# Kernel tuning notes

Measured on AMD Instinct MI355X. Metric: run time of the kernel, lower is better.

The kernel has to match this reference:

```python
import jax, jax.numpy as jnp
from jax import lax
import numpy as np

B, DIM, L_IN = 8, 512, 4096
SCALE = 2
KSIZE = 17
DN = ('NCH', 'OIH', 'NCH')  # conv1d dimension numbers


def _aa_kernel(kernel_size: int, scale: int) -> np.ndarray:
    # replicates scipy.signal.kaiser_atten / kaiser_beta / windows.kaiser
    atten = 2.285 * (kernel_size - 1) * np.pi * (1.0 / scale) + 7.95
    if atten > 50:
        beta = 0.1102 * (atten - 8.7)
    elif atten > 21:
        beta = 0.5842 * (atten - 21) ** 0.4 + 0.07886 * (atten - 21)
    else:
        beta = 0.0
    win = np.kaiser(kernel_size, beta)
    xk = np.arange(kernel_size) - kernel_size // 2
    k = np.sinc(xk / scale) * win  # normalized sinc, same as torch.sinc
    return (k / k.sum()).astype(np.float32)


def setup_inputs() -> dict:
    key = jax.random.key(0)
    k1, k2, k3, k4, k5 = jax.random.split(key, 5)
    kconv = 2 * SCALE - 1
    return {
        'x': jax.random.normal(k1, (B, DIM, L_IN), dtype=jnp.float32),
        'conv_w': jax.random.normal(k2, (DIM, DIM, kconv), dtype=jnp.float32) * (1.0 / np.sqrt(DIM * kconv)),
        'conv_b': jax.random.normal(k3, (DIM,), dtype=jnp.float32) * 0.01,
        'aa_kernel': jnp.asarray(_aa_kernel(KSIZE, SCALE)),
        'proj_w': jax.random.normal(k4, (DIM, DIM), dtype=jnp.float32) * (1.0 / np.sqrt(DIM)),
        'proj_b': jax.random.normal(k5, (DIM,), dtype=jnp.float32) * 0.01,
    }


def reference(x, conv_w, conv_b, aa_kernel, proj_w, proj_b):
    s = SCALE
    # zero-insertion upsample + Conv1d(dim,dim,2s-1,pad=s-1) fused via lhs_dilation.
    # Torch zero-inserts to length l*s (trailing s-1 zeros), so right pad is 2s-2.
    y = lax.conv_general_dilated(
        x, conv_w, window_strides=(1,), padding=[(s - 1, 2 * s - 2)],
        lhs_dilation=(s,), dimension_numbers=DN,
    ) + conv_b[None, :, None]  # [B, D, l*s]
    # depthwise anti-alias filter (same Kaiser-sinc kernel per channel)
    dw = jnp.broadcast_to(aa_kernel, (DIM, 1, KSIZE))
    y = lax.conv_general_dilated(
        y, dw, window_strides=(1,), padding=[(KSIZE // 2, KSIZE // 2)],
        feature_group_count=DIM, dimension_numbers=DN,
    )
    # pointwise 1x1 projection
    return jnp.einsum('bdl,ed->bel', y, proj_w) + proj_b[None, :, None]
```

## Files before the change

kernel.cpp:

```cpp
#include <hip/hip_runtime.h>
#include <hip/hip_bf16.h>

#define BB_   8
#define DIM_  512
#define LIN_  4096
#define LOUT_ 8192

typedef __attribute__((ext_vector_type(8))) __bf16 bf16x8;
typedef __attribute__((ext_vector_type(4))) float  f32x4;
typedef __attribute__((ext_vector_type(8))) unsigned short u16x8;

__device__ __forceinline__ float bf2f(unsigned short u) {
  union { unsigned int i; float f; } x;
  x.i = ((unsigned int)u) << 16;
  return x.f;
}

__device__ __forceinline__ unsigned short f2bf(float f) {
  unsigned int u = __float_as_uint(f);
  return (unsigned short)((u + 0x7fffu + ((u >> 16) & 1u)) >> 16);
}

__device__ __forceinline__ void gload16(const void* g, void* l) {
  __builtin_amdgcn_global_load_lds(
      (__attribute__((address_space(1))) void*)(g),
      (__attribute__((address_space(3))) void*)(l), 16, 0, 0);
}

__global__ __launch_bounds__(256) void k_prep(const float* __restrict__ proj_w,
                                              const float* __restrict__ conv_w,
                                              const float* __restrict__ conv_b,
                                              const float* __restrict__ x,
                                              unsigned short* __restrict__ Mst,
                                              float* __restrict__ Pcb,
                                              unsigned short* __restrict__ Xbt) {
  __shared__ __align__(16) float sm[4160];
  const int bx  = blockIdx.x;
  const int tid = threadIdx.x;

  if (bx < 192) {
    float* Pt = sm;
    float* Wt = sm + 1088;
    const int kk = bx >> 6;
    const int t6 = bx & 63;
    const int et = (t6 >> 3) << 6;
    const int it = (t6 & 7) << 6;
    const int tx = tid & 15, ty = tid >> 4;
    const int le = tid & 63, lg = tid >> 6;
    float acc[4][4] = {};
    for (int d0 = 0; d0 < DIM_; d0 += 16) {
      {
        const float4 v = *(const float4*)&proj_w[(size_t)(et + le) * DIM_ + d0 + lg * 4];
        Pt[(lg * 4 + 0) * 68 + le] = v.x;
        Pt[(lg * 4 + 1) * 68 + le] = v.y;
        Pt[(lg * 4 + 2) * 68 + le] = v.z;
        Pt[(lg * 4 + 3) * 68 + le] = v.w;
      }
#pragma unroll
      for (int r = 0; r < 4; ++r) {
        const int dl = r * 4 + lg;
        Wt[dl * 68 + le] = conv_w[(size_t)(d0 + dl) * (DIM_ * 3) + (it + le) * 3 + kk];
      }
      __syncthreads();
#pragma unroll
      for (int dl = 0; dl < 16; ++dl) {
        const float4 pv = *(const float4*)&Pt[dl * 68 + ty * 4];
        const float4 wv = *(const float4*)&Wt[dl * 68 + tx * 4];
        const float pa[4] = {pv.x, pv.y, pv.z, pv.w};
        const float wa[4] = {wv.x, wv.y, wv.z, wv.w};
#pragma unroll
        for (int a = 0; a < 4; ++a)
#pragma unroll
          for (int b = 0; b < 4; ++b) acc[a][b] += pa[a] * wa[b];
      }
      __syncthreads();
    }
#pragma unroll
    for (int a = 0; a < 4; ++a) {
      uint2 pk;
      pk.x = (unsigned int)f2bf(acc[a][0]) | ((unsigned int)f2bf(acc[a][1]) << 16);
      pk.y = (unsigned int)f2bf(acc[a][2]) | ((unsigned int)f2bf(acc[a][3]) << 16);
      *(uint2*)&Mst[(size_t)(kk * DIM_ + et + ty * 4 + a) * DIM_ + it + tx * 4] = pk;
    }
  } else if (bx < 320) {
    const int idx = bx - 192;
    const int e = idx * 4 + (tid >> 6);
    const int j = tid & 63;
    float s = 0.f;
#pragma unroll
    for (int d = j; d < DIM_; d += 64) s += proj_w[(size_t)e * DIM_ + d] * conv_b[d];
#pragma unroll
    for (int off = 32; off > 0; off >>= 1) s += __shfl_down(s, off, 64);
    if (j == 0) Pcb[e] = s;
  } else {
    const int bc = bx - 320;
    const int bb = bc >> 9;
    const int dt = ((bc >> 6) & 7) << 6;
    const int lt = (bc & 63) << 6;
    const int lr  = tid >> 4;
    const int lc4 = (tid & 15) << 2;
#pragma unroll
    for (int r = 0; r < 4; ++r) {
      const int d = r * 16 + lr;
      const float4 v = *(const float4*)&x[((size_t)(bb * DIM_ + dt + d) << 12) + lt + lc4];
      float* row = sm + d * 65 + lc4;
      row[0] = v.x; row[1] = v.y; row[2] = v.z; row[3] = v.w;
    }
    __syncthreads();
#pragma unroll
    for (int rr = 0; rr < 2; ++rr) {
      const int flat = rr * 256 + tid;
      const int l  = flat >> 3;
      const int d8 = (flat & 7) << 3;
      unsigned int w[4];
#pragma unroll
      for (int p = 0; p < 4; ++p) {
        const float f0 = sm[(d8 + 2 * p + 0) * 65 + l];
        const float f1 = sm[(d8 + 2 * p + 1) * 65 + l];
        w[p] = (unsigned int)f2bf(f0) | ((unsigned int)f2bf(f1) << 16);
      }
      uint4 pk; pk.x = w[0]; pk.y = w[1]; pk.z = w[2]; pk.w = w[3];
      *(uint4*)&Xbt[((size_t)(bb * LIN_ + lt + l) << 9) + dt + d8] = pk;
    }
  }
}

__global__ __launch_bounds__(512, 2) void k_gemm(const unsigned short* __restrict__ Xbt,
                                                 const unsigned short* __restrict__ Mst,
                                                 const float* __restrict__ Pcb,
                                                 unsigned short* __restrict__ U) {
  __shared__ __align__(16) char lds[131072];
  const int tid = threadIdx.x;
  const int bid = blockIdx.x;
  const int wgs   = (bid & 7) * 96 + (bid >> 3);
  const int ntile = wgs / 6;
  const int mtile = wgs - ntile * 6;
  const int bb = ntile >> 4;
  const int l0 = (ntile & 15) << 8;
  const int m0 = mtile << 8;

  const int srow   = tid >> 2;
  const int schunk = (tid & 3) ^ ((srow >> 1) & 3);
  const unsigned short* Ag = Mst + (size_t)(m0 + srow) * 512 + schunk * 8;
  const unsigned short* Bg = Xbt + ((size_t)(bb * LIN_ + l0 + srow) << 9) + schunk * 8;
  char* ldsw = lds + (tid >> 6) * 1024;

#define STAGE_(kt_, buf_)                          \
  do {                                             \
    const unsigned short* ga_ = Ag + (kt_) * 32;   \
    const unsigned short* gb_ = Bg + (kt_) * 32;   \
    char* la_ = ldsw + (buf_) * 32768;             \
    gload16(ga_,         la_);                     \
    gload16(ga_ + 65536, la_ + 8192);              \
    gload16(gb_,         la_ + 16384);             \
    gload16(gb_ + 65536, la_ + 24576);             \
  } while (0)

  const int lane = tid & 63;
  const int wave = tid >> 6;
  const int wm = wave >> 2;
  const int wn = wave & 3;
  const int lrow = lane & 15;
  const int lc   = lane >> 4;
  const int aslot = lc ^ ((lrow >> 1) & 3);
  const char* ldsA0 = lds + ((wm * 128 + lrow) * 64 + aslot * 16);
  const char* ldsB0 = lds + (16384 + (wn * 64 + lrow) * 64 + aslot * 16);

  f32x4 acc[8][4] = {};

  STAGE_(0, 0); STAGE_(1, 1); STAGE_(2, 2);

#pragma unroll 4
  for (int kt = 0; kt < 16; ++kt) {
    if (kt < 13) STAGE_(kt + 3, (kt + 3) & 3);
    if (kt < 13)       asm volatile("s_waitcnt vmcnt(12)" ::: "memory");
    else if (kt == 13) asm volatile("s_waitcnt vmcnt(8)" ::: "memory");
    else if (kt == 14) asm volatile("s_waitcnt vmcnt(4)" ::: "memory");
    else               asm volatile("s_waitcnt vmcnt(0)" ::: "memory");
    __builtin_amdgcn_s_barrier();
    __builtin_amdgcn_sched_barrier(0);

    const int bo = (kt & 3) * 32768;
    bf16x8 af[8], bfr[4];
#pragma unroll
    for (int mt = 0; mt < 8; ++mt) af[mt] = *(const bf16x8*)(ldsA0 + bo + mt * 1024);
#pragma unroll
    for (int nt = 0; nt < 4; ++nt) bfr[nt] = *(const bf16x8*)(ldsB0 + bo + nt * 1024);
#pragma unroll
    for (int mt = 0; mt < 8; ++mt)
#pragma unroll
      for (int nt = 0; nt < 4; ++nt)
        acc[mt][nt] = __builtin_amdgcn_mfma_f32_16x16x32_bf16(bfr[nt], af[mt],
                                                              acc[mt][nt], 0, 0, 0);
    asm volatile("s_waitcnt lgkmcnt(0)" ::: "memory");
    __builtin_amdgcn_sched_barrier(0);
    __builtin_amdgcn_s_barrier();
  }
#undef STAGE_

  const int es0 = m0 + wm * 128 + lrow;
  const int lq  = l0 + wn * 64 + (lc << 2);
#pragma unroll
  for (int mt = 0; mt < 8; ++mt) {
    const int es = es0 + mt * 16;
    const int kk = es >> 9;
    const int e  = es & 511;
    const float bias = (kk < 2) ? Pcb[e] : 0.f;
    unsigned short* urow = U + (((size_t)((kk * 8 + bb) * 512 + e)) << 12) + lq;
#pragma unroll
    for (int nt = 0; nt < 4; ++nt) {
      uint2 pk;
      pk.x = (unsigned int)f2bf(acc[mt][nt][0] + bias) |
             ((unsigned int)f2bf(acc[mt][nt][1] + bias) << 16);
      pk.y = (unsigned int)f2bf(acc[mt][nt][2] + bias) |
             ((unsigned int)f2bf(acc[mt][nt][3] + bias) << 16);
      *(uint2*)(urow + nt * 16) = pk;
    }
  }
}

__global__ __launch_bounds__(256) void k_aa(const __hip_bfloat16* __restrict__ U,
                                            const float* __restrict__ aa,
                                            const float* __restrict__ proj_b,
                                            float* __restrict__ out) {
  const int b  = blockIdx.x >> 9;
  const int e  = blockIdx.x & 511;
  const int l0 = blockIdx.y << 11;
  const int tid = threadIdx.x;
  const int lt = l0 + 8 * tid;
  const unsigned short* q0 = (const unsigned short*)(U + (size_t)((0 * 8 + b) * 512 + e) * 4096);
  const unsigned short* q1 = (const unsigned short*)(U + (size_t)((1 * 8 + b) * 512 + e) * 4096);
  const unsigned short* q2 = (const unsigned short*)(U + (size_t)((2 * 8 + b) * 512 + e) * 4096);

  float E[17], O[16];
  if (lt >= 8 && lt + 16 <= 4096) {
    const int base = lt - 8;
    unsigned short r1[24], r0[24], r2[24];
#pragma unroll
    for (int c = 0; c < 3; ++c) {
      const u16x8 a = *(const u16x8*)(q1 + base + 8 * c);
      const u16x8 d = *(const u16x8*)(q0 + base + 8 * c);
      const u16x8 g = *(const u16x8*)(q2 + base + 8 * c);
#pragma unroll
      for (int j = 0; j < 8; ++j) {
        r1[8 * c + j] = a[j]; r0[8 * c + j] = d[j]; r2[8 * c + j] = g[j];
      }
    }
#pragma unroll
    for (int j = 0; j < 17; ++j) E[j] = bf2f(r1[4 + j]);
#pragma unroll
    for (int j = 0; j < 16; ++j) O[j] = bf2f(r0[4 + j]) + bf2f(r2[5 + j]);
  } else {
#pragma unroll
    for (int j = 0; j < 17; ++j) {
      const int l = lt - 4 + j;
      E[j] = (l >= 0 && l < 4096) ? bf2f(q1[l]) : 0.f;
    }
#pragma unroll
    for (int j = 0; j < 16; ++j) {
      const int l = lt - 4 + j;
      float v = 0.f;
      if (l >= 0 && l < 4096) {
        v = bf2f(q0[l]);
        if (l + 1 < 4096) v += bf2f(q2[l + 1]);
      }
      O[j] = v;
    }
  }

  float sa[17];
#pragma unroll
  for (int j = 0; j < 17; ++j) sa[j] = aa[j];
  const float pb = proj_b[e];
  float res[16];
#pragma unroll
  for (int t = 0; t < 8; ++t) {
    float se = 0.f, so = 0.f;
#pragma unroll
    for (int q = 0; q <= 8; ++q) {
      se += sa[2 * q] * E[t + q];
      so += sa[2 * q] * O[t + q];
    }
#pragma unroll
    for (int q = 0; q < 8; ++q) {
      se += sa[2 * q + 1] * O[t + q];
      so += sa[2 * q + 1] * E[t + q + 1];
    }
    res[2 * t]     = se + pb;
    res[2 * t + 1] = so + pb;
  }
  float* orow = out + (size_t)(b * 512 + e) * 8192 + 2 * lt;
#pragma unroll
  for (int c = 0; c < 4; ++c)
    *(float4*)(orow + 4 * c) = *(const float4*)&res[4 * c];
}

extern "C" void kernel_launch(void* const* d_in, const int* in_sizes, int n_in,
                              void* d_out, int out_size, void* d_ws, size_t ws_size,
                              hipStream_t stream) {
  const float* x      = (const float*)d_in[0];
  const float* conv_w = (const float*)d_in[1];
  const float* conv_b = (const float*)d_in[2];
  const float* aa     = (const float*)d_in[3];
  const float* proj_w = (const float*)d_in[4];
  const float* proj_b = (const float*)d_in[5];
  float* out = (float*)d_out;

  char* ws = (char*)d_ws;
  unsigned short* Mst = (unsigned short*)ws;
  float*          Pcb = (float*)(ws + 1572864);
  unsigned short* Xbt = (unsigned short*)(ws + 1574912);
  unsigned short* U   = (unsigned short*)(ws + 35129344);

  k_prep<<<dim3(4416, 1, 1), 256, 0, stream>>>(proj_w, conv_w, conv_b, x, Mst, Pcb, Xbt);
  k_gemm<<<dim3(768, 1, 1), 512, 0, stream>>>(Xbt, Mst, Pcb, U);
  k_aa<<<dim3(4096, 2), 256, 0, stream>>>((const __hip_bfloat16*)U, aa, proj_b, out);
}
```

Baseline: 344.3 us.

## Fuse GEMM and anti-alias filter via LDS-resident halo tiles

The separate GEMM and depthwise-filter kernels are merged into one. Each workgroup now computes a 192x288 output tile, covering three kernel taps for 64 channels over 256 positions plus a 32-column halo, and keeps the bf16 result in LDS. The filter then reads from LDS instead of a global intermediate U buffer. This removes the write and re-read of the large bf16 intermediate and one kernel launch. In exchange the GEMM tile shape changes and about 12% of the B-side loads and MMA work is spent recomputing halo columns.

```diff
diff --git a/kernel.cpp b/kernel.cpp
--- a/kernel.cpp
+++ b/kernel.cpp
@@ -125,72 +125,97 @@
   }
 }
 
-__global__ __launch_bounds__(512, 2) void k_gemm(const unsigned short* __restrict__ Xbt,
-                                                 const unsigned short* __restrict__ Mst,
-                                                 const float* __restrict__ Pcb,
-                                                 unsigned short* __restrict__ U) {
+__global__ __launch_bounds__(512, 2) void k_fused(const unsigned short* __restrict__ Xbt,
+                                                  const unsigned short* __restrict__ Mst,
+                                                  const float* __restrict__ Pcb,
+                                                  const float* __restrict__ aa,
+                                                  const float* __restrict__ proj_b,
+                                                  float* __restrict__ out) {
   __shared__ __align__(16) char lds[131072];
   const int tid = threadIdx.x;
   const int bid = blockIdx.x;
-  const int wgs   = (bid & 7) * 96 + (bid >> 3);
-  const int ntile = wgs / 6;
-  const int mtile = wgs - ntile * 6;
+  const int wgs   = (bid & 7) * 128 + (bid >> 3);
+  const int ntile = wgs >> 3;
+  const int etile = wgs & 7;
   const int bb = ntile >> 4;
-  const int l0 = (ntile & 15) << 8;
-  const int m0 = mtile << 8;
-
-  const int srow   = tid >> 2;
-  const int schunk = (tid & 3) ^ ((srow >> 1) & 3);
-  const unsigned short* Ag = Mst + (size_t)(m0 + srow) * 512 + schunk * 8;
-  const unsigned short* Bg = Xbt + ((size_t)(bb * LIN_ + l0 + srow) << 9) + schunk * 8;
-  char* ldsw = lds + (tid >> 6) * 1024;
-
-#define STAGE_(kt_, buf_)                          \
-  do {                                             \
-    const unsigned short* ga_ = Ag + (kt_) * 32;   \
-    const unsigned short* gb_ = Bg + (kt_) * 32;   \
-    char* la_ = ldsw + (buf_) * 32768;             \
-    gload16(ga_,         la_);                     \
-    gload16(ga_ + 65536, la_ + 8192);              \
-    gload16(gb_,         la_ + 16384);             \
-    gload16(gb_ + 65536, la_ + 24576);             \
+  const int L0 = (ntile & 15) << 8;
+  const int l0g = L0 - 16;
+  const int e0 = etile << 6;
+
+  const int wave = tid >> 6;
+  const int lane = tid & 63;
+
+  const unsigned short* src[4];
+  int ldso[4];
+#pragma unroll
+  for (int i = 0; i < 4; ++i) {
+    const int u  = wave + 8 * i;
+    const int uu = (u >= 30) ? (u - 30) : u;
+    const int rl = lane >> 2;
+    const int sl = lane & 3;
+    int row;
+    const unsigned short* p;
+    if (uu < 12) {
+      row = uu * 16 + rl;
+      const int kk = uu >> 2;
+      const int er = e0 + ((uu & 3) << 4) + rl;
+      p = Mst + ((long long)(kk * 512 + er) << 9);
+    } else {
+      const int lr = (uu - 12) * 16 + rl;
+      row = lr;
+      p = Xbt + ((long long)(bb * LIN_) + (l0g + lr)) * 512;
+    }
+    src[i] = p + ((sl ^ ((row >> 1) & 3)) << 3);
+    ldso[i] = u << 10;
+  }
+
+#define STAGE_(kt_, buf_)                              \
+  do {                                                 \
+    char* base_ = lds + (buf_) * 32768;                \
+    gload16(src[0] + (kt_) * 32, base_ + ldso[0]);     \
+    gload16(src[1] + (kt_) * 32, base_ + ldso[1]);     \
+    gload16(src[2] + (kt_) * 32, base_ + ldso[2]);     \
+    gload16(src[3] + (kt_) * 32, base_ + ldso[3]);     \
   } while (0)
 
-  const int lane = tid & 63;
-  const int wave = tid >> 6;
-  const int wm = wave >> 2;
-  const int wn = wave & 3;
+  const int wm = wave >> 1;
+  const int wn = wave & 1;
   const int lrow = lane & 15;
   const int lc   = lane >> 4;
-  const int aslot = lc ^ ((lrow >> 1) & 3);
-  const char* ldsA0 = lds + ((wm * 128 + lrow) * 64 + aslot * 16);
-  const char* ldsB0 = lds + (16384 + (wn * 64 + lrow) * 64 + aslot * 16);
-
-  f32x4 acc[8][4] = {};
+  const int asl  = lc ^ ((lrow >> 1) & 3);
+  const char* A0 = lds + ((wm * 48 + lrow) * 64 + asl * 16);
+  const char* B0 = lds + (12288 + (wn * 144 + lrow) * 64 + asl * 16);
+
+  f32x4 acc[3][9] = {};
 
   STAGE_(0, 0); STAGE_(1, 1); STAGE_(2, 2);
 
 #pragma unroll 4
   for (int kt = 0; kt < 16; ++kt) {
-    if (kt < 13) STAGE_(kt + 3, (kt + 3) & 3);
-    if (kt < 13)       asm volatile("s_waitcnt vmcnt(12)" ::: "memory");
-    else if (kt == 13) asm volatile("s_waitcnt vmcnt(8)" ::: "memory");
-    else if (kt == 14) asm volatile("s_waitcnt vmcnt(4)" ::: "memory");
-    else               asm volatile("s_waitcnt vmcnt(0)" ::: "memory");
+    if (kt < 13) {
+      STAGE_(kt + 3, (kt + 3) & 3);
+      asm volatile("s_waitcnt vmcnt(12)" ::: "memory");
+    } else if (kt == 13) {
+      asm volatile("s_waitcnt vmcnt(8)" ::: "memory");
+    } else if (kt == 14) {
+      asm volatile("s_waitcnt vmcnt(4)" ::: "memory");
+    } else {
+      asm volatile("s_waitcnt vmcnt(0)" ::: "memory");
+    }
     __builtin_amdgcn_s_barrier();
     __builtin_amdgcn_sched_barrier(0);
 
     const int bo = (kt & 3) * 32768;
-    bf16x8 af[8], bfr[4];
-#pragma unroll
-    for (int mt = 0; mt < 8; ++mt) af[mt] = *(const bf16x8*)(ldsA0 + bo + mt * 1024);
-#pragma unroll
-    for (int nt = 0; nt < 4; ++nt) bfr[nt] = *(const bf16x8*)(ldsB0 + bo + nt * 1024);
-#pragma unroll
-    for (int mt = 0; mt < 8; ++mt)
-#pragma unroll
-      for (int nt = 0; nt < 4; ++nt)
-        acc[mt][nt] = __builtin_amdgcn_mfma_f32_16x16x32_bf16(bfr[nt], af[mt],
+    bf16x8 af[3], bfv[9];
+#pragma unroll
+    for (int mt = 0; mt < 3; ++mt) af[mt] = *(const bf16x8*)(A0 + bo + mt * 1024);
+#pragma unroll
+    for (int nt = 0; nt < 9; ++nt) bfv[nt] = *(const bf16x8*)(B0 + bo + nt * 1024);
+#pragma unroll
+    for (int mt = 0; mt < 3; ++mt)
+#pragma unroll
+      for (int nt = 0; nt < 9; ++nt)
+        acc[mt][nt] = __builtin_amdgcn_mfma_f32_16x16x32_bf16(bfv[nt], af[mt],
                                                               acc[mt][nt], 0, 0, 0);
     asm volatile("s_waitcnt lgkmcnt(0)" ::: "memory");
     __builtin_amdgcn_sched_barrier(0);
@@ -198,101 +223,99 @@
   }
 #undef STAGE_
 
-  const int es0 = m0 + wm * 128 + lrow;
-  const int lq  = l0 + wn * 64 + (lc << 2);
-#pragma unroll
-  for (int mt = 0; mt < 8; ++mt) {
-    const int es = es0 + mt * 16;
-    const int kk = es >> 9;
-    const int e  = es & 511;
-    const float bias = (kk < 2) ? Pcb[e] : 0.f;
-    unsigned short* urow = U + (((size_t)((kk * 8 + bb) * 512 + e)) << 12) + lq;
-#pragma unroll
-    for (int nt = 0; nt < 4; ++nt) {
+  unsigned short* Ut = (unsigned short*)lds;
+#pragma unroll
+  for (int mt = 0; mt < 3; ++mt) {
+    const int m = wm * 48 + mt * 16 + lrow;
+#pragma unroll
+    for (int nt = 0; nt < 9; ++nt) {
+      const int lcol = wn * 144 + nt * 16 + (lc << 2);
       uint2 pk;
-      pk.x = (unsigned int)f2bf(acc[mt][nt][0] + bias) |
-             ((unsigned int)f2bf(acc[mt][nt][1] + bias) << 16);
-      pk.y = (unsigned int)f2bf(acc[mt][nt][2] + bias) |
-             ((unsigned int)f2bf(acc[mt][nt][3] + bias) << 16);
-      *(uint2*)(urow + nt * 16) = pk;
-    }
-  }
-}
-
-__global__ __launch_bounds__(256) void k_aa(const __hip_bfloat16* __restrict__ U,
-                                            const float* __restrict__ aa,
-                                            const float* __restrict__ proj_b,
-                                            float* __restrict__ out) {
-  const int b  = blockIdx.x >> 9;
-  const int e  = blockIdx.x & 511;
-  const int l0 = blockIdx.y << 11;
-  const int tid = threadIdx.x;
-  const int lt = l0 + 8 * tid;
-  const unsigned short* q0 = (const unsigned short*)(U + (size_t)((0 * 8 + b) * 512 + e) * 4096);
-  const unsigned short* q1 = (const unsigned short*)(U + (size_t)((1 * 8 + b) * 512 + e) * 4096);
-  const unsigned short* q2 = (const unsigned short*)(U + (size_t)((2 * 8 + b) * 512 + e) * 4096);
-
-  float E[17], O[16];
-  if (lt >= 8 && lt + 16 <= 4096) {
-    const int base = lt - 8;
-    unsigned short r1[24], r0[24], r2[24];
-#pragma unroll
-    for (int c = 0; c < 3; ++c) {
-      const u16x8 a = *(const u16x8*)(q1 + base + 8 * c);
-      const u16x8 d = *(const u16x8*)(q0 + base + 8 * c);
-      const u16x8 g = *(const u16x8*)(q2 + base + 8 * c);
+      pk.x = (unsigned int)f2bf(acc[mt][nt][0]) | ((unsigned int)f2bf(acc[mt][nt][1]) << 16);
+      pk.y = (unsigned int)f2bf(acc[mt][nt][2]) | ((unsigned int)f2bf(acc[mt][nt][3]) << 16);
+      *(uint2*)&Ut[m * 296 + lcol] = pk;
+    }
+  }
+  __syncthreads();
+
+  const int el  = tid >> 3;
+  const int lt0 = (tid & 7) << 5;
+  const int e   = e0 + el;
+  const float pcb = Pcb[e];
+  const float pb  = proj_b[e];
+  float sa[17];
+#pragma unroll
+  for (int j = 0; j < 17; ++j) sa[j] = aa[j];
+  const unsigned short* u0r = Ut + (size_t)el * 296;
+  const unsigned short* u1r = Ut + (size_t)(64 + el) * 296;
+  const unsigned short* u2r = Ut + (size_t)(128 + el) * 296;
+  const bool edge = (L0 == 0) || (L0 == 3840);
+  float* orow = out + (((size_t)(bb * 512 + e)) << 13) + 2 * (size_t)(L0 + lt0);
+
+#pragma unroll
+  for (int cc = 0; cc < 4; ++cc) {
+    const int c0 = lt0 + 8 * cc + 12;
+    float E[17], O[16];
+    if (!edge) {
+      const u16x8 e0v = *(const u16x8*)(u1r + c0 - 4);
+      const u16x8 e1v = *(const u16x8*)(u1r + c0 + 4);
+      const u16x8 e2v = *(const u16x8*)(u1r + c0 + 12);
+      const u16x8 a0v = *(const u16x8*)(u0r + c0 - 4);
+      const u16x8 a1v = *(const u16x8*)(u0r + c0 + 4);
+      const u16x8 a2v = *(const u16x8*)(u0r + c0 + 12);
+      const u16x8 b0v = *(const u16x8*)(u2r + c0 - 4);
+      const u16x8 b1v = *(const u16x8*)(u2r + c0 + 4);
+      const u16x8 b2v = *(const u16x8*)(u2r + c0 + 12);
+      unsigned short ue[24], ua[24], ub[24];
 #pragma unroll
       for (int j = 0; j < 8; ++j) {
-        r1[8 * c + j] = a[j]; r0[8 * c + j] = d[j]; r2[8 * c + j] = g[j];
-      }
-    }
-#pragma unroll
-    for (int j = 0; j < 17; ++j) E[j] = bf2f(r1[4 + j]);
-#pragma unroll
-    for (int j = 0; j < 16; ++j) O[j] = bf2f(r0[4 + j]) + bf2f(r2[5 + j]);
-  } else {
-#pragma unroll
-    for (int j = 0; j < 17; ++j) {
-      const int l = lt - 4 + j;
-      E[j] = (l >= 0 && l < 4096) ? bf2f(q1[l]) : 0.f;
-    }
-#pragma unroll
-    for (int j = 0; j < 16; ++j) {
-      const int l = lt - 4 + j;
-      float v = 0.f;
-      if (l >= 0 && l < 4096) {
-        v = bf2f(q0[l]);
-        if (l + 1 < 4096) v += bf2f(q2[l + 1]);
-      }
-      O[j] = v;
-    }
-  }
-
-  float sa[17];
-#pragma unroll
-  for (int j = 0; j < 17; ++j) sa[j] = aa[j];
-  const float pb = proj_b[e];
-  float res[16];
-#pragma unroll
-  for (int t = 0; t < 8; ++t) {
-    float se = 0.f, so = 0.f;
-#pragma unroll
-    for (int q = 0; q <= 8; ++q) {
-      se += sa[2 * q] * E[t + q];
-      so += sa[2 * q] * O[t + q];
-    }
-#pragma unroll
-    for (int q = 0; q < 8; ++q) {
-      se += sa[2 * q + 1] * O[t + q];
-      so += sa[2 * q + 1] * E[t + q + 1];
-    }
-    res[2 * t]     = se + pb;
-    res[2 * t + 1] = so + pb;
-  }
-  float* orow = out + (size_t)(b * 512 + e) * 8192 + 2 * lt;
-#pragma unroll
-  for (int c = 0; c < 4; ++c)
-    *(float4*)(orow + 4 * c) = *(const float4*)&res[4 * c];
+        ue[j] = e0v[j]; ue[j + 8] = e1v[j]; ue[j + 16] = e2v[j];
+        ua[j] = a0v[j]; ua[j + 8] = a1v[j]; ua[j + 16] = a2v[j];
+        ub[j] = b0v[j]; ub[j + 8] = b1v[j]; ub[j + 16] = b2v[j];
+      }
+#pragma unroll
+      for (int j = 0; j < 17; ++j) E[j] = bf2f(ue[4 + j]) + pcb;
+#pragma unroll
+      for (int j = 0; j < 16; ++j) O[j] = bf2f(ua[4 + j]) + pcb + bf2f(ub[5 + j]);
+    } else {
+      const int lt = L0 + lt0 + 8 * cc;
+#pragma unroll
+      for (int j = 0; j < 17; ++j) {
+        const int l = lt - 4 + j;
+        E[j] = (l >= 0 && l < 4096) ? (bf2f(u1r[c0 + j]) + pcb) : 0.f;
+      }
+#pragma unroll
+      for (int j = 0; j < 16; ++j) {
+        const int l = lt - 4 + j;
+        float v = 0.f;
+        if (l >= 0 && l < 4096) {
+          v = bf2f(u0r[c0 + j]) + pcb;
+          if (l + 1 < 4096) v += bf2f(u2r[c0 + j + 1]);
+        }
+        O[j] = v;
+      }
+    }
+    float res[16];
+#pragma unroll
+    for (int t = 0; t < 8; ++t) {
+      float se = 0.f, so = 0.f;
+#pragma unroll
+      for (int q = 0; q <= 8; ++q) {
+        se += sa[2 * q] * E[t + q];
+        so += sa[2 * q] * O[t + q];
+      }
+#pragma unroll
+      for (int q = 0; q < 8; ++q) {
+        se += sa[2 * q + 1] * O[t + q];
+        so += sa[2 * q + 1] * E[t + q + 1];
+      }
+      res[2 * t]     = se + pb;
+      res[2 * t + 1] = so + pb;
+    }
+#pragma unroll
+    for (int c2 = 0; c2 < 4; ++c2)
+      *(float4*)(orow + 16 * cc + 4 * c2) = *(const float4*)&res[4 * c2];
+  }
 }
 
 extern "C" void kernel_launch(void* const* d_in, const int* in_sizes, int n_in,
@@ -310,9 +333,7 @@
   unsigned short* Mst = (unsigned short*)ws;
   float*          Pcb = (float*)(ws + 1572864);
   unsigned short* Xbt = (unsigned short*)(ws + 1574912);
-  unsigned short* U   = (unsigned short*)(ws + 35129344);
 
   k_prep<<<dim3(4416, 1, 1), 256, 0, stream>>>(proj_w, conv_w, conv_b, x, Mst, Pcb, Xbt);
-  k_gemm<<<dim3(768, 1, 1), 512, 0, stream>>>(Xbt, Mst, Pcb, U);
-  k_aa<<<dim3(4096, 2), 256, 0, stream>>>((const __hip_bfloat16*)U, aa, proj_b, out);
-}
+  k_fused<<<dim3(1024, 1, 1), 512, 0, stream>>>(Xbt, Mst, Pcb, aa, proj_b, out);
+}
```

Result: faster. 321.9 us (-6.5%).
